# Kernel tuning notes

Hardware: AMD Instinct MI355X
Metric: run time of the kernel (lower is better)

## Reference

```python
import jax, jax.numpy as jnp
import numpy as np


def setup_inputs() -> dict:
    key = jax.random.key(0)
    k1, k2, k3, k4 = jax.random.split(key, 4)
    B_, T, I = 32, 512, 1024
    L, H = 2, 1024
    scale = 0.05  # keep activations in a sane range for sigmoid/tanh
    return {
        "sequence": jax.random.normal(k1, (B_, T, I), dtype=jnp.float32),
        # gate order along axis 1: [forget(Wf), input-gate(Ww), candidate(Wi), output(Wc)]
        "Wh": jax.random.normal(k2, (L, 4, H, H), dtype=jnp.float32) * scale,
        "Wx": jax.random.normal(k3, (L, 4, H, I), dtype=jnp.float32) * scale,
        "B": jax.random.normal(k4, (L, 4, H), dtype=jnp.float32) * scale,
    }


def reference(sequence, Wh, Wx, B):
    # sequence: [batch, seq_len, input]; Wh/Wx: [L, 4, H, H/I]; B: [L, 4, H]
    batch = sequence.shape[0]
    L, _, H, _ = Wh.shape
    c0 = jnp.zeros((L, batch, H), dtype=sequence.dtype)
    h0 = jnp.zeros((L, batch, H), dtype=sequence.dtype)

    def step(carry, x_t):
        c, h = carry  # each [L, batch, H]
        cs, hs = [], []
        x = x_t  # [batch, input]
        for l in range(L):  # small structural loop over layers
            # gates[:, g] = h @ Wh[l,g].T + x @ Wx[l,g].T + B[l,g]  (matches torch einsum 'xy,ay->ax')
            gates = (jnp.einsum('ghd,bd->bgh', Wh[l], h[l])
                     + jnp.einsum('ghd,bd->bgh', Wx[l], x)
                     + B[l])  # [batch, 4, H]
            f, w, i, o = gates[:, 0], gates[:, 1], gates[:, 2], gates[:, 3]
            c_new = c[l] * jax.nn.sigmoid(f) + jax.nn.sigmoid(w) * jnp.tanh(i)
            h_new = jnp.tanh(c_new) * jax.nn.sigmoid(o)
            cs.append(c_new)
            hs.append(h_new)
            x = h_new  # next layer consumes this layer's hidden
        return (jnp.stack(cs), jnp.stack(hs)), None

    (c_fin, h_fin), _ = jax.lax.scan(step, (c0, h0), jnp.swapaxes(sequence, 0, 1))
    return h_fin[-1]  # final-timestep hidden of last layer: [batch, H]
```

## Files before the change

### kernel.cpp

```cpp
#include <hip/hip_runtime.h>

#define T_STEPS 512
#define HID 1024
#define SEQ_BSTRIDE (T_STEPS * HID)

#define WL 0
#define WSTR 20
#define ZL 5120
#define ZSTR 36
#define GLB 4608
#define LDS_DW 14336

__launch_bounds__(256, 1)
__global__ void lstm_step(const float* __restrict__ seq,
                          const float* __restrict__ Wh,
                          const float* __restrict__ Wx,
                          const float* __restrict__ Bias,
                          float* __restrict__ Ht,
                          float* __restrict__ C,
                          float* __restrict__ dout,
                          int t, int l, int write_out)
{
    __shared__ float lds[LDS_DW];
    const int tid = threadIdx.x;
    const int bid = blockIdx.x;

    const int kg   = tid >> 3;
    const int rowg = (tid >> 2) & 1;
    const int bg   = tid & 3;

    const int pIn = t & 1, pOut = pIn ^ 1;
    const float* zh   = Ht + ((pIn * 2 + l) << 15);
    const float* zx_d = Ht + ((pOut * 2) << 15);
    float* hOut = Ht + ((pOut * 2 + l) << 15);
    float* cPtr = C + (l << 15);

    const int srow = tid >> 4;
    const int skv  = tid & 15;
    const int sdv  = tid >> 3;
    const int sb4  = tid & 7;
    const int sb   = tid >> 3;
    const int sd8  = tid & 7;

    const float* whbase = Wh + ((size_t)(((l * 4 + (srow >> 2)) << 10) + (bid << 2) + (srow & 3))) * 1024;
    const float* wxbase = Wx + ((size_t)(((l * 4 + (srow >> 2)) << 10) + (bid << 2) + (srow & 3))) * 1024;

    float4 pfw[4];
    float4 pfz[8];

    auto LOADC = [&](int c) {
        const float* wb = (c < 4) ? (whbase + c * 256) : (wxbase + (c - 4) * 256);
        #pragma unroll
        for (int j = 0; j < 4; ++j)
            pfw[j] = *(const float4*)(wb + j * 64 + skv * 4);
        if (c < 4) {
            const float* zsrc = zh + (c << 8) * 32;
            #pragma unroll
            for (int j = 0; j < 8; ++j)
                pfz[j] = *(const float4*)(zsrc + (j * 32 + sdv) * 32 + sb4 * 4);
        } else if (l == 1) {
            const float* zsrc = zx_d + ((c - 4) << 8) * 32;
            #pragma unroll
            for (int j = 0; j < 8; ++j)
                pfz[j] = *(const float4*)(zsrc + (j * 32 + sdv) * 32 + sb4 * 4);
        } else {
            const float* xs = seq + (size_t)sb * SEQ_BSTRIDE + t * HID + (c - 4) * 256;
            #pragma unroll
            for (int j = 0; j < 8; ++j)
                pfz[j] = *(const float4*)(xs + j * 32 + sd8 * 4);
        }
    };

    auto WRITEC = [&](int c) {
        #pragma unroll
        for (int j = 0; j < 4; ++j) {
            const int kk = j * 64 + skv * 4;
            lds[WL + (kk + 0) * WSTR + srow] = pfw[j].x;
            lds[WL + (kk + 1) * WSTR + srow] = pfw[j].y;
            lds[WL + (kk + 2) * WSTR + srow] = pfw[j].z;
            lds[WL + (kk + 3) * WSTR + srow] = pfw[j].w;
        }
        if (c < 4 || l == 1) {
            #pragma unroll
            for (int j = 0; j < 8; ++j)
                *(float4*)&lds[ZL + (j * 32 + sdv) * ZSTR + sb4 * 4] = pfz[j];
        } else {
            #pragma unroll
            for (int j = 0; j < 8; ++j) {
                const int dd = j * 32 + sd8 * 4;
                lds[ZL + (dd + 0) * ZSTR + sb] = pfz[j].x;
                lds[ZL + (dd + 1) * ZSTR + sb] = pfz[j].y;
                lds[ZL + (dd + 2) * ZSTR + sb] = pfz[j].z;
                lds[ZL + (dd + 3) * ZSTR + sb] = pfz[j].w;
            }
        }
    };

    float4 acc[8][2];
    #pragma unroll
    for (int r = 0; r < 8; ++r) {
        acc[r][0] = make_float4(0.f, 0.f, 0.f, 0.f);
        acc[r][1] = make_float4(0.f, 0.f, 0.f, 0.f);
    }

    LOADC(0);
    WRITEC(0);
    __syncthreads();

    const int wbase = WL + kg * WSTR + rowg * 8;
    const int zbase = ZL + kg * ZSTR + bg * 8;

    for (int c = 0; c < 8; ++c) {
        if (c < 7) LOADC(c + 1);

        #pragma unroll
        for (int i = 0; i < 8; ++i) {
            const float* wp = &lds[wbase + i * (32 * WSTR)];
            const float* zp = &lds[zbase + i * (32 * ZSTR)];
            const float4 wa  = *(const float4*)(wp);
            const float4 wb2 = *(const float4*)(wp + 4);
            const float4 za  = *(const float4*)(zp);
            const float4 zb2 = *(const float4*)(zp + 4);
            const float wr[8] = {wa.x, wa.y, wa.z, wa.w, wb2.x, wb2.y, wb2.z, wb2.w};
            #pragma unroll
            for (int r = 0; r < 8; ++r) {
                acc[r][0].x = fmaf(wr[r], za.x,  acc[r][0].x);
                acc[r][0].y = fmaf(wr[r], za.y,  acc[r][0].y);
                acc[r][0].z = fmaf(wr[r], za.z,  acc[r][0].z);
                acc[r][0].w = fmaf(wr[r], za.w,  acc[r][0].w);
                acc[r][1].x = fmaf(wr[r], zb2.x, acc[r][1].x);
                acc[r][1].y = fmaf(wr[r], zb2.y, acc[r][1].y);
                acc[r][1].z = fmaf(wr[r], zb2.z, acc[r][1].z);
                acc[r][1].w = fmaf(wr[r], zb2.w, acc[r][1].w);
            }
        }

        __syncthreads();
        if (c < 7) {
            WRITEC(c + 1);
            __syncthreads();
        }
    }

    #pragma unroll
    for (int r = 0; r < 8; ++r) {
        #pragma unroll
        for (int q = 0; q < 2; ++q) {
            float4 v = acc[r][q];
            v.x += __shfl_xor(v.x, 8);  v.y += __shfl_xor(v.y, 8);
            v.z += __shfl_xor(v.z, 8);  v.w += __shfl_xor(v.w, 8);
            v.x += __shfl_xor(v.x, 16); v.y += __shfl_xor(v.y, 16);
            v.z += __shfl_xor(v.z, 16); v.w += __shfl_xor(v.w, 16);
            v.x += __shfl_xor(v.x, 32); v.y += __shfl_xor(v.y, 32);
            v.z += __shfl_xor(v.z, 32); v.w += __shfl_xor(v.w, 32);
            acc[r][q] = v;
        }
    }

    const int wv = tid >> 6;
    if ((tid & 56) == 0) {
        #pragma unroll
        for (int r = 0; r < 8; ++r) {
            const float vals[8] = {acc[r][0].x, acc[r][0].y, acc[r][0].z, acc[r][0].w,
                                   acc[r][1].x, acc[r][1].y, acc[r][1].z, acc[r][1].w};
            #pragma unroll
            for (int b2 = 0; b2 < 8; ++b2) {
                const int o  = ((rowg * 8 + r) << 5) + bg * 8 + b2;
                const int sw = ((o >> 3) & 3) * 4 + ((o >> 8) & 1) * 16;
                lds[o * 8 + sw + wv] = vals[b2];
            }
        }
    }
    __syncthreads();

    #pragma unroll
    for (int ii = 0; ii < 2; ++ii) {
        const int o  = tid + ii * 256;
        const int sw = ((o >> 3) & 3) * 4 + ((o >> 8) & 1) * 16;
        const float4 p = *(const float4*)&lds[o * 8 + sw];
        float s = p.x + p.y + p.z + p.w;
        const int row = o >> 5;
        const int g = row >> 2, hl = row & 3;
        s += Bias[((l * 4 + g) << 10) + (bid << 2) + hl];
        lds[GLB + o] = s;
    }
    __syncthreads();

    if (tid < 128) {
        const int hl = tid >> 5, b = tid & 31;
        const float gf = lds[GLB + (0 * 4 + hl) * 32 + b];
        const float gw = lds[GLB + (1 * 4 + hl) * 32 + b];
        const float gi = lds[GLB + (2 * 4 + hl) * 32 + b];
        const float go = lds[GLB + (3 * 4 + hl) * 32 + b];
        const int h = (bid << 2) + hl;
        const int sidx = (h << 5) + b;
        const float c_old = cPtr[sidx];
        const float sf = 1.f / (1.f + __expf(-gf));
        const float sw2 = 1.f / (1.f + __expf(-gw));
        const float ti = tanhf(gi);
        const float so = 1.f / (1.f + __expf(-go));
        const float c_new = c_old * sf + sw2 * ti;
        const float h_new = tanhf(c_new) * so;
        cPtr[sidx] = c_new;
        hOut[sidx] = h_new;
        if (write_out) dout[b * HID + h] = h_new;
    }
}

extern "C" void kernel_launch(void* const* d_in, const int* in_sizes, int n_in,
                              void* d_out, int out_size, void* d_ws, size_t ws_size,
                              hipStream_t stream) {
    const float* seq  = (const float*)d_in[0];
    const float* Wh   = (const float*)d_in[1];
    const float* Wx   = (const float*)d_in[2];
    const float* Bias = (const float*)d_in[3];

    float* Ht = (float*)d_ws;
    float* C  = Ht + 131072;
    hipMemsetAsync(d_ws, 0, (size_t)(131072 + 65536) * sizeof(float), stream);

    for (int t = 0; t < T_STEPS; ++t) {
        for (int l = 0; l < 2; ++l) {
            const int wo = (t == T_STEPS - 1 && l == 1) ? 1 : 0;
            lstm_step<<<dim3(256), dim3(256), 0, stream>>>(
                seq, Wh, Wx, Bias, Ht, C, (float*)d_out, t, l, wo);
        }
    }
}
```

Measured before the change: 28.95 ms.

## Replace per-step launches with persistent cooperative kernel pipelining both layers

Replaces the 1024 sequential kernel launches with one cooperative persistent kernel of 512 blocks, half per layer, synchronized by grid.sync each step. Layer 1 runs one timestep behind layer 0, so both layers compute concurrently and only 513 grid barriers are needed. Cell state stays in registers, bias is preloaded, and LDS tiles are halved and XOR-swizzled to allow two blocks per CU. It trades launch overhead for grid-barrier cost, and falls back to the old per-step launches if the cooperative launch fails.

```diff
diff --git a/kernel.cpp b/kernel.cpp
--- a/kernel.cpp
+++ b/kernel.cpp
@@ -1,27 +1,248 @@
 #include <hip/hip_runtime.h>
+#include <hip/hip_cooperative_groups.h>
+
+namespace cg = cooperative_groups;
 
 #define T_STEPS 512
 #define HID 1024
 #define SEQ_BSTRIDE (T_STEPS * HID)
 
-#define WL 0
-#define WSTR 20
-#define ZL 5120
-#define ZSTR 36
-#define GLB 4608
-#define LDS_DW 14336
+#define P_WSTR 20
+#define P_ZL   2560
+#define P_ZSTR 36
+#define P_GLB  4608
+#define P_LDS  7168
+
+__launch_bounds__(256, 2)
+__global__ void lstm_persist(const float* __restrict__ seq,
+                             const float* __restrict__ Wh,
+                             const float* __restrict__ Wx,
+                             const float* __restrict__ Bias,
+                             float* __restrict__ Ht,
+                             float* __restrict__ dout)
+{
+    cg::grid_group grid = cg::this_grid();
+    __shared__ float lds[P_LDS];
+
+    const int tid   = threadIdx.x;
+    const int blk   = blockIdx.x;
+    const int layer = blk & 1;
+    const int hblk  = blk >> 1;
+
+    const int kg   = tid >> 3;
+    const int rowg = (tid >> 2) & 1;
+    const int bg   = tid & 3;
+
+    const int srow = tid >> 4, skv = tid & 15;
+    const int sdv  = tid >> 3, sb4 = tid & 7;
+    const int sbb  = tid >> 3, sd8 = tid & 7;
+
+    const float* whbase = Wh + (size_t)(((layer*4 + (srow>>2))<<10) + (hblk<<2) + (srow&3)) * 1024;
+    const float* wxbase = Wx + (size_t)(((layer*4 + (srow>>2))<<10) + (hblk<<2) + (srow&3)) * 1024;
+
+    const int swzW = ((kg>>3)&3) << 2;
+    const int rA   = (rowg<<3) ^ swzW;
+    const int wrb1 = kg*P_WSTR + rA;
+    const int wrb2 = kg*P_WSTR + (rA^4);
+
+    float c_reg = 0.f;
+    const int act_hl = tid>>5, act_b = tid&31;
+    float bf_=0.f, bw_=0.f, bi_=0.f, bo_=0.f;
+    if (tid < 128) {
+        const int h = (hblk<<2) + act_hl;
+        bf_ = Bias[((layer*4+0)<<10) + h];
+        bw_ = Bias[((layer*4+1)<<10) + h];
+        bi_ = Bias[((layer*4+2)<<10) + h];
+        bo_ = Bias[((layer*4+3)<<10) + h];
+    }
+
+    for (int p = 0; p <= T_STEPS; ++p) {
+        const int t = layer ? (p-1) : p;
+        if (t >= 0 && t < T_STEPS) {
+            const int pIn = t & 1, pOut = pIn ^ 1;
+            const float* zh   = Ht + ((pIn*2 + layer) << 15);
+            const float* zx_d = Ht + ((pOut*2) << 15);
+            const float* xseq = seq + (size_t)t * HID;
+            float* hOut = Ht + ((pOut*2 + layer) << 15);
+
+            float4 pfw0, pfw1, pfz[4];
+
+            auto LOADC = [&](int c) {
+                const float* wb = (c < 8) ? (whbase + (c<<7)) : (wxbase + ((c-8)<<7));
+                pfw0 = *(const float4*)(wb + (skv<<3));
+                pfw1 = *(const float4*)(wb + (skv<<3) + 4);
+                if (c < 8 || layer == 1) {
+                    const float* zsrc = (c < 8) ? (zh + (c<<12)) : (zx_d + ((c-8)<<12));
+                    #pragma unroll
+                    for (int j = 0; j < 4; ++j)
+                        pfz[j] = *(const float4*)(zsrc + (((j<<5)+sdv)<<5) + (sb4<<2));
+                } else {
+                    const float* xs = xseq + (size_t)sbb * SEQ_BSTRIDE + ((c-8)<<7) + (sd8<<4);
+                    #pragma unroll
+                    for (int j = 0; j < 4; ++j)
+                        pfz[j] = *(const float4*)(xs + (j<<2));
+                }
+            };
+
+            auto WRITEC = [&](int c) {
+                const int rs = srow ^ ((skv&3)<<2);
+                const int kb = skv<<3;
+                lds[(kb+0)*P_WSTR + rs] = pfw0.x;
+                lds[(kb+1)*P_WSTR + rs] = pfw0.y;
+                lds[(kb+2)*P_WSTR + rs] = pfw0.z;
+                lds[(kb+3)*P_WSTR + rs] = pfw0.w;
+                lds[(kb+4)*P_WSTR + rs] = pfw1.x;
+                lds[(kb+5)*P_WSTR + rs] = pfw1.y;
+                lds[(kb+6)*P_WSTR + rs] = pfw1.z;
+                lds[(kb+7)*P_WSTR + rs] = pfw1.w;
+                if (c < 8 || layer == 1) {
+                    #pragma unroll
+                    for (int j = 0; j < 4; ++j) {
+                        const int d   = (j<<5) + sdv;
+                        const int swz = ((d>>4)&7) << 2;
+                        *(float4*)&lds[P_ZL + d*P_ZSTR + ((sb4<<2) ^ swz)] = pfz[j];
+                    }
+                } else {
+                    const int bcol = sbb ^ (sd8<<2);
+                    #pragma unroll
+                    for (int j = 0; j < 4; ++j) {
+                        const int d0 = (sd8<<4) + (j<<2);
+                        lds[P_ZL + (d0+0)*P_ZSTR + bcol] = pfz[j].x;
+                        lds[P_ZL + (d0+1)*P_ZSTR + bcol] = pfz[j].y;
+                        lds[P_ZL + (d0+2)*P_ZSTR + bcol] = pfz[j].z;
+                        lds[P_ZL + (d0+3)*P_ZSTR + bcol] = pfz[j].w;
+                    }
+                }
+            };
+
+            float4 acc[8][2];
+            #pragma unroll
+            for (int r = 0; r < 8; ++r) {
+                acc[r][0] = make_float4(0.f,0.f,0.f,0.f);
+                acc[r][1] = make_float4(0.f,0.f,0.f,0.f);
+            }
+
+            LOADC(0);
+            WRITEC(0);
+            __syncthreads();
+
+            for (int c = 0; c < 16; ++c) {
+                if (c < 15) LOADC(c + 1);
+
+                #pragma unroll
+                for (int i = 0; i < 4; ++i) {
+                    const int kk = i << 5;
+                    const float4 wa  = *(const float4*)&lds[wrb1 + kk*P_WSTR];
+                    const float4 wb2 = *(const float4*)&lds[wrb2 + kk*P_WSTR];
+                    const int swzZ = (((kg>>4) + 2*i) & 7) << 2;
+                    const int zb   = P_ZL + (kg + kk)*P_ZSTR;
+                    const int boff = (bg<<3) ^ swzZ;
+                    const float4 za = *(const float4*)&lds[zb + boff];
+                    const float4 zc = *(const float4*)&lds[zb + (boff^4)];
+                    const float wr[8] = {wa.x,wa.y,wa.z,wa.w, wb2.x,wb2.y,wb2.z,wb2.w};
+                    #pragma unroll
+                    for (int r = 0; r < 8; ++r) {
+                        acc[r][0].x = fmaf(wr[r], za.x, acc[r][0].x);
+                        acc[r][0].y = fmaf(wr[r], za.y, acc[r][0].y);
+                        acc[r][0].z = fmaf(wr[r], za.z, acc[r][0].z);
+                        acc[r][0].w = fmaf(wr[r], za.w, acc[r][0].w);
+                        acc[r][1].x = fmaf(wr[r], zc.x, acc[r][1].x);
+                        acc[r][1].y = fmaf(wr[r], zc.y, acc[r][1].y);
+                        acc[r][1].z = fmaf(wr[r], zc.z, acc[r][1].z);
+                        acc[r][1].w = fmaf(wr[r], zc.w, acc[r][1].w);
+                    }
+                }
+
+                __syncthreads();
+                if (c < 15) {
+                    WRITEC(c + 1);
+                    __syncthreads();
+                }
+            }
+
+            #pragma unroll
+            for (int r = 0; r < 8; ++r) {
+                #pragma unroll
+                for (int q = 0; q < 2; ++q) {
+                    float4 v = acc[r][q];
+                    v.x += __shfl_xor(v.x, 8);  v.y += __shfl_xor(v.y, 8);
+                    v.z += __shfl_xor(v.z, 8);  v.w += __shfl_xor(v.w, 8);
+                    v.x += __shfl_xor(v.x, 16); v.y += __shfl_xor(v.y, 16);
+                    v.z += __shfl_xor(v.z, 16); v.w += __shfl_xor(v.w, 16);
+                    v.x += __shfl_xor(v.x, 32); v.y += __shfl_xor(v.y, 32);
+                    v.z += __shfl_xor(v.z, 32); v.w += __shfl_xor(v.w, 32);
+                    acc[r][q] = v;
+                }
+            }
+
+            const int wv = tid >> 6;
+            if ((tid & 56) == 0) {
+                #pragma unroll
+                for (int r = 0; r < 8; ++r) {
+                    const float vals[8] = {acc[r][0].x, acc[r][0].y, acc[r][0].z, acc[r][0].w,
+                                           acc[r][1].x, acc[r][1].y, acc[r][1].z, acc[r][1].w};
+                    #pragma unroll
+                    for (int b2 = 0; b2 < 8; ++b2) {
+                        const int o  = ((rowg * 8 + r) << 5) + bg * 8 + b2;
+                        const int sw = ((o >> 3) & 3) * 4 + ((o >> 8) & 1) * 16;
+                        lds[o * 8 + sw + wv] = vals[b2];
+                    }
+                }
+            }
+            __syncthreads();
+
+            #pragma unroll
+            for (int ii = 0; ii < 2; ++ii) {
+                const int o  = tid + (ii << 8);
+                const int sw = ((o >> 3) & 3) * 4 + ((o >> 8) & 1) * 16;
+                const float4 pq = *(const float4*)&lds[o * 8 + sw];
+                lds[P_GLB + o] = pq.x + pq.y + pq.z + pq.w;
+            }
+            __syncthreads();
+
+            if (tid < 128) {
+                const float gf = lds[P_GLB + (0*4 + act_hl)*32 + act_b] + bf_;
+                const float gw = lds[P_GLB + (1*4 + act_hl)*32 + act_b] + bw_;
+                const float gi = lds[P_GLB + (2*4 + act_hl)*32 + act_b] + bi_;
+                const float go = lds[P_GLB + (3*4 + act_hl)*32 + act_b] + bo_;
+                const int h    = (hblk<<2) + act_hl;
+                const int sidx = (h<<5) + act_b;
+                const float sf  = 1.f / (1.f + __expf(-gf));
+                const float sw2 = 1.f / (1.f + __expf(-gw));
+                const float ti  = tanhf(gi);
+                const float so  = 1.f / (1.f + __expf(-go));
+                const float c_new = c_reg * sf + sw2 * ti;
+                const float h_new = tanhf(c_new) * so;
+                c_reg = c_new;
+                hOut[sidx] = h_new;
+                if (layer == 1 && t == T_STEPS - 1)
+                    dout[act_b * HID + h] = h_new;
+            }
+            __syncthreads();
+        }
+
+        __threadfence();
+        grid.sync();
+    }
+}
+
+#define F_WSTR 20
+#define F_ZL 5120
+#define F_ZSTR 36
+#define F_GLB 4608
+#define F_LDS 14336
 
 __launch_bounds__(256, 1)
-__global__ void lstm_step(const float* __restrict__ seq,
-                          const float* __restrict__ Wh,
-                          const float* __restrict__ Wx,
-                          const float* __restrict__ Bias,
-                          float* __restrict__ Ht,
-                          float* __restrict__ C,
-                          float* __restrict__ dout,
-                          int t, int l, int write_out)
+__global__ void lstm_step_fb(const float* __restrict__ seq,
+                             const float* __restrict__ Wh,
+                             const float* __restrict__ Wx,
+                             const float* __restrict__ Bias,
+                             float* __restrict__ Ht,
+                             float* __restrict__ C,
+                             float* __restrict__ dout,
+                             int t, int l, int write_out)
 {
-    __shared__ float lds[LDS_DW];
+    __shared__ float lds[F_LDS];
     const int tid = threadIdx.x;
     const int bid = blockIdx.x;
 
@@ -75,23 +296,23 @@
         #pragma unroll
         for (int j = 0; j < 4; ++j) {
             const int kk = j * 64 + skv * 4;
-            lds[WL + (kk + 0) * WSTR + srow] = pfw[j].x;
-            lds[WL + (kk + 1) * WSTR + srow] = pfw[j].y;
-            lds[WL + (kk + 2) * WSTR + srow] = pfw[j].z;
-            lds[WL + (kk + 3) * WSTR + srow] = pfw[j].w;
+            lds[(kk + 0) * F_WSTR + srow] = pfw[j].x;
+            lds[(kk + 1) * F_WSTR + srow] = pfw[j].y;
+            lds[(kk + 2) * F_WSTR + srow] = pfw[j].z;
+            lds[(kk + 3) * F_WSTR + srow] = pfw[j].w;
         }
         if (c < 4 || l == 1) {
             #pragma unroll
             for (int j = 0; j < 8; ++j)
-                *(float4*)&lds[ZL + (j * 32 + sdv) * ZSTR + sb4 * 4] = pfz[j];
+                *(float4*)&lds[F_ZL + (j * 32 + sdv) * F_ZSTR + sb4 * 4] = pfz[j];
         } else {
             #pragma unroll
             for (int j = 0; j < 8; ++j) {
                 const int dd = j * 32 + sd8 * 4;
-                lds[ZL + (dd + 0) * ZSTR + sb] = pfz[j].x;
-                lds[ZL + (dd + 1) * ZSTR + sb] = pfz[j].y;
-                lds[ZL + (dd + 2) * ZSTR + sb] = pfz[j].z;
-                lds[ZL + (dd + 3) * ZSTR + sb] = pfz[j].w;
+                lds[F_ZL + (dd + 0) * F_ZSTR + sb] = pfz[j].x;
+                lds[F_ZL + (dd + 1) * F_ZSTR + sb] = pfz[j].y;
+                lds[F_ZL + (dd + 2) * F_ZSTR + sb] = pfz[j].z;
+                lds[F_ZL + (dd + 3) * F_ZSTR + sb] = pfz[j].w;
             }
         }
     };
@@ -107,16 +328,16 @@
     WRITEC(0);
     __syncthreads();
 
-    const int wbase = WL + kg * WSTR + rowg * 8;
-    const int zbase = ZL + kg * ZSTR + bg * 8;
+    const int wbase = kg * F_WSTR + rowg * 8;
+    const int zbase = F_ZL + kg * F_ZSTR + bg * 8;
 
     for (int c = 0; c < 8; ++c) {
         if (c < 7) LOADC(c + 1);
 
         #pragma unroll
         for (int i = 0; i < 8; ++i) {
-            const float* wp = &lds[wbase + i * (32 * WSTR)];
-            const float* zp = &lds[zbase + i * (32 * ZSTR)];
+            const float* wp = &lds[wbase + i * (32 * F_WSTR)];
+            const float* zp = &lds[zbase + i * (32 * F_ZSTR)];
             const float4 wa  = *(const float4*)(wp);
             const float4 wb2 = *(const float4*)(wp + 4);
             const float4 za  = *(const float4*)(zp);
@@ -177,21 +398,21 @@
     for (int ii = 0; ii < 2; ++ii) {
         const int o  = tid + ii * 256;
         const int sw = ((o >> 3) & 3) * 4 + ((o >> 8) & 1) * 16;
-        const float4 p = *(const float4*)&lds[o * 8 + sw];
-        float s = p.x + p.y + p.z + p.w;
+        const float4 pq = *(const float4*)&lds[o * 8 + sw];
+        float s = pq.x + pq.y + pq.z + pq.w;
         const int row = o >> 5;
         const int g = row >> 2, hl = row & 3;
         s += Bias[((l * 4 + g) << 10) + (bid << 2) + hl];
-        lds[GLB + o] = s;
+        lds[F_GLB + o] = s;
     }
     __syncthreads();
 
     if (tid < 128) {
         const int hl = tid >> 5, b = tid & 31;
-        const float gf = lds[GLB + (0 * 4 + hl) * 32 + b];
-        const float gw = lds[GLB + (1 * 4 + hl) * 32 + b];
-        const float gi = lds[GLB + (2 * 4 + hl) * 32 + b];
-        const float go = lds[GLB + (3 * 4 + hl) * 32 + b];
+        const float gf = lds[F_GLB + (0 * 4 + hl) * 32 + b];
+        const float gw = lds[F_GLB + (1 * 4 + hl) * 32 + b];
+        const float gi = lds[F_GLB + (2 * 4 + hl) * 32 + b];
+        const float go = lds[F_GLB + (3 * 4 + hl) * 32 + b];
         const int h = (bid << 2) + hl;
         const int sidx = (h << 5) + b;
         const float c_old = cPtr[sidx];
@@ -214,16 +435,23 @@
     const float* Wh   = (const float*)d_in[1];
     const float* Wx   = (const float*)d_in[2];
     const float* Bias = (const float*)d_in[3];
-
-    float* Ht = (float*)d_ws;
-    float* C  = Ht + 131072;
+    float* Ht   = (float*)d_ws;
+    float* C    = Ht + 131072;
+    float* dout = (float*)d_out;
+
     hipMemsetAsync(d_ws, 0, (size_t)(131072 + 65536) * sizeof(float), stream);
 
-    for (int t = 0; t < T_STEPS; ++t) {
-        for (int l = 0; l < 2; ++l) {
-            const int wo = (t == T_STEPS - 1 && l == 1) ? 1 : 0;
-            lstm_step<<<dim3(256), dim3(256), 0, stream>>>(
-                seq, Wh, Wx, Bias, Ht, C, (float*)d_out, t, l, wo);
+    void* args[] = {(void*)&seq, (void*)&Wh, (void*)&Wx, (void*)&Bias,
+                    (void*)&Ht, (void*)&dout};
+    hipError_t err = hipLaunchCooperativeKernel((const void*)lstm_persist,
+                                                dim3(512), dim3(256), args, 0, stream);
+    if (err != hipSuccess) {
+        for (int t = 0; t < T_STEPS; ++t) {
+            for (int l = 0; l < 2; ++l) {
+                const int wo = (t == T_STEPS - 1 && l == 1) ? 1 : 0;
+                lstm_step_fb<<<dim3(256), dim3(256), 0, stream>>>(
+                    seq, Wh, Wx, Bias, Ht, C, dout, t, l, wo);
+            }
         }
     }
 }
```

New measurement: 57.30 ms. +97.9%, slower.
